# Kernel tuning notes

Hardware: AMD Instinct MI355X
Metric: run time of the kernel (lower is better)

The kernel has to match this reference:

```python
import jax, jax.numpy as jnp
import numpy as np

H = 16        # num_heads
E = 1024      # embed_size
OUT = 1024    # out_dim
TEMP = 1.0
EPS = 1e-20
LN_EPS = 1e-5


def setup_inputs() -> dict:
    key = jax.random.key(0)
    ks = jax.random.split(key, 16)
    B, S = 8, 4096
    s = 1.0 / np.sqrt(E)
    inp = {
        'x': jax.random.normal(ks[0], (B, S, E), dtype=jnp.float32),
        'gumbel_u': jax.random.uniform(ks[1], (B, H, S, 2), dtype=jnp.float32, minval=1e-6, maxval=1.0 - 1e-6),
        'query': jax.random.uniform(ks[2], (1, E), dtype=jnp.float32, minval=-s, maxval=s),  # xavier-ish
        'Wq': jax.random.uniform(ks[3], (E, E), jnp.float32, -s, s),
        'bq': jnp.zeros((E,), jnp.float32),
        'Wk': jax.random.uniform(ks[4], (E, E), jnp.float32, -s, s),
        'bk': jnp.zeros((E,), jnp.float32),
        'Wv': jax.random.uniform(ks[5], (E, E), jnp.float32, -s, s),
        'bv': jnp.zeros((E,), jnp.float32),
        'ln_g': jnp.ones((E,), jnp.float32),
        'ln_b': jnp.zeros((E,), jnp.float32),
        'W1': jax.random.uniform(ks[6], (4 * E, E), jnp.float32, -s, s),
        'b1': jnp.zeros((4 * E,), jnp.float32),
        'W2': jax.random.uniform(ks[7], (OUT, 4 * E), jnp.float32, -0.5 * s, 0.5 * s),
        'b2': jnp.zeros((OUT,), jnp.float32),
    }
    return inp


def reference(x, gumbel_u, query, Wq, bq, Wk, bk, Wv, bv, ln_g, ln_b, W1, b1, W2, b2):
    B, S, _ = x.shape
    dk = E // H
    # projections
    q = (query @ Wq.T + bq).reshape(H, dk)                      # [H, dk] (single query, broadcast over batch)
    k = (x @ Wk.T + bk).reshape(B, S, H, dk)                    # [B, S, H, dk]
    v = (x @ Wv.T + bv).reshape(B, S, H, dk)
    # single-query attention logits
    logits = jnp.einsum('hd,bshd->bhs', q, k) / np.sqrt(dk)     # [B, H, S]
    probs = jax.nn.softmax(logits, axis=-1)                     # [B, H, S]
    # gumbel-softmax hard mask over {keep=0-logit, drop/keep pair}
    edges = jnp.stack([jnp.zeros_like(logits), logits], axis=-1)  # [B, H, S, 2]
    g = -jnp.log(-jnp.log(gumbel_u + EPS) + EPS)
    y_soft = jax.nn.softmax((edges + g) / TEMP, axis=-1)
    idx = jnp.argmax(y_soft, axis=-1)
    y_hard = jax.nn.one_hot(idx, 2, dtype=y_soft.dtype)
    y = jax.lax.stop_gradient(y_hard - y_soft) + y_soft         # straight-through
    A = y[..., 1]                                               # [B, H, S]
    probs = A * probs
    # weighted sum of values; merge heads (seq_len of query is 1)
    hidden = jnp.einsum('bhs,bshd->bhd', probs, v).reshape(B, E)
    # layernorm
    mu = hidden.mean(axis=-1, keepdims=True)
    var = hidden.var(axis=-1, keepdims=True)
    hidden = (hidden - mu) / jnp.sqrt(var + LN_EPS) * ln_g + ln_b
    # MLP (dropout p=0 -> identity)
    out = jax.nn.relu(hidden @ W1.T + b1) @ W2.T + b2           # [B, OUT]
    masks = A.sum(axis=1)[:, None, :]                           # sum_heads=True -> [B, 1, S]
    attn = probs.sum(axis=1)[:, None, :]
    return out, masks, attn
```

## Files before the change

kernel.cpp:

```cpp
#include <hip/hip_runtime.h>
#include <hip/hip_bf16.h>
#include <math.h>

#define SS 4096
#define EE 1024
#define HH 16

typedef __bf16 bf16x8 __attribute__((ext_vector_type(8)));
typedef float  f32x4v __attribute__((ext_vector_type(4)));

#define OFF_QVEC 0L
#define OFF_QKB  1024L
#define OFF_QH   1040L
#define OFF_QL   9232L
#define OFF_SEC  17424L
#define OFF_SAC  50192L
#define OFF_INVD 82960L
#define OFF_PSUM 83088L
#define OFF_WG   83216L
#define OFF_XA   607504L
#define OFF_HID  738576L
#define OFF_H2   746768L
#define OFF_T1   754960L
#define OFF_PT   787728L
#define OFF_PX   820496L

__device__ __forceinline__ float bf2f(unsigned int u){
  union { unsigned int i; float f; } c; c.i = u << 16; return c.f;
}
__device__ __forceinline__ unsigned int pk_hi(float a, float b){
  return __builtin_amdgcn_perm(__float_as_uint(b), __float_as_uint(a), 0x07060302u);
}
__device__ __forceinline__ float lo_part(float f){
  return f - __uint_as_float(__float_as_uint(f) & 0xFFFF0000u);
}
__device__ __forceinline__ unsigned short f2bf_rn(float f){
  unsigned int u = __float_as_uint(f);
  return (unsigned short)((u + 0x7fffu + ((u >> 16) & 1u)) >> 16);
}
__device__ __forceinline__ f32x4v mfma16(bf16x8 a, bf16x8 b, f32x4v c){
  return __builtin_amdgcn_mfma_f32_16x16x32_bf16(a, b, c, 0, 0, 0);
}
__device__ __forceinline__ float waveRedSum(float v){
  #pragma unroll
  for (int m=1;m<64;m<<=1) v += __shfl_xor(v, m, 64);
  return v;
}
template<int NW>
__device__ __forceinline__ float blockRedSum(float v, volatile float* scr){
  v = waveRedSum(v);
  const int w = threadIdx.x >> 6;
  __syncthreads();
  if ((threadIdx.x & 63) == 0) scr[w] = v;
  __syncthreads();
  float r = 0.f;
  #pragma unroll
  for (int i=0;i<NW;i++) r += scr[i];
  return r;
}

__global__ __launch_bounds__(256) void k1(const float* __restrict__ query, const float* __restrict__ Wq,
                                          const float* __restrict__ bq, float* __restrict__ qvec){
  const int wv = threadIdx.x >> 6, lane = threadIdx.x & 63;
  const int j = blockIdx.x * 4 + wv;
  float p = 0.f;
  #pragma unroll
  for (int i=0;i<4;i++){
    const int e = 4*lane + 256*i;
    const float4 q4 = *(const float4*)(query + e);
    const float4 w4 = *(const float4*)(Wq + (long)j*EE + e);
    p += q4.x*w4.x + q4.y*w4.y + q4.z*w4.z + q4.w*w4.w;
  }
  p = waveRedSum(p);
  if (lane == 0) qvec[j] = p + bq[j];
}

__global__ __launch_bounds__(256) void k2(const float* __restrict__ Wk, const float* __restrict__ bk,
                                          const float* __restrict__ qvec,
                                          unsigned short* __restrict__ qh, unsigned short* __restrict__ ql,
                                          float* __restrict__ qkb){
  __shared__ float red[4][64];
  const int wv = threadIdx.x >> 6, lane = threadIdx.x & 63;
  const int h = blockIdx.y;
  const int e = blockIdx.x*64 + lane;
  float acc = 0.f;
  #pragma unroll
  for (int dd=0; dd<16; dd++){
    const int d = wv*16 + dd;
    acc += qvec[h*64+d] * Wk[(long)(h*64+d)*EE + e];
  }
  red[wv][lane] = acc;
  __syncthreads();
  if (wv == 0){
    const float s = red[0][lane] + red[1][lane] + red[2][lane] + red[3][lane];
    const unsigned int ub = __float_as_uint(s);
    qh[h*EE + e] = (unsigned short)(ub >> 16);
    const float lo = s - __uint_as_float(ub & 0xFFFF0000u);
    ql[h*EE + e] = (unsigned short)(__float_as_uint(lo) >> 16);
    if (blockIdx.x == 0){
      float p = qvec[h*64+lane] * bk[h*64+lane];
      p = waveRedSum(p);
      if (lane == 0) qkb[h] = p;
    }
  }
}

__global__ __launch_bounds__(256,2) void k3(const float* __restrict__ x, const float* __restrict__ gum,
                                            const unsigned short* __restrict__ qh, const unsigned short* __restrict__ ql,
                                            const float* __restrict__ qkb,
                                            float* __restrict__ seC, float* __restrict__ saC,
                                            float* __restrict__ Wg, float* __restrict__ out){
  __shared__ float lg[4*16*17];
  __shared__ float w[16*20];
  __shared__ float scrA[16*17], scrB[16*17];
  __shared__ float sQkb[16];
  const int t = threadIdx.x;
  const int wv = t >> 6, lane = t & 63;
  const int m16 = lane & 15, q = lane >> 4;
  const int c = blockIdx.x, b = blockIdx.y;
  if (t < 16) sQkb[t] = qkb[t];
  const long xbase = ((long)(b*SS + c*16))*EE;

  f32x4v a = {0.f,0.f,0.f,0.f};
  #pragma unroll
  for (int kt=0; kt<8; kt++){
    const int k = wv*256 + kt*32 + q*8;
    const float* xp = x + xbase + (long)m16*EE + k;
    const float4 f0 = *(const float4*)(xp);
    const float4 f1 = *(const float4*)(xp + 4);
    union { uint4 u; bf16x8 v; } xh, xl, bh, bl;
    xh.u.x = pk_hi(f0.x, f0.y); xh.u.y = pk_hi(f0.z, f0.w);
    xh.u.z = pk_hi(f1.x, f1.y); xh.u.w = pk_hi(f1.z, f1.w);
    xl.u.x = pk_hi(lo_part(f0.x), lo_part(f0.y)); xl.u.y = pk_hi(lo_part(f0.z), lo_part(f0.w));
    xl.u.z = pk_hi(lo_part(f1.x), lo_part(f1.y)); xl.u.w = pk_hi(lo_part(f1.z), lo_part(f1.w));
    bh.u = *(const uint4*)(qh + (long)m16*EE + k);
    bl.u = *(const uint4*)(ql + (long)m16*EE + k);
    a = mfma16(xh.v, bh.v, a);
    a = mfma16(xh.v, bl.v, a);
    a = mfma16(xl.v, bh.v, a);
  }
  #pragma unroll
  for (int r=0;r<4;r++)
    lg[(wv*16 + q*4 + r)*17 + m16] = a[r];
  __syncthreads();

  {
    const int h = t & 15, s = t >> 4;
    const float dot = lg[(0*16+s)*17+h] + lg[(1*16+s)*17+h]
                    + lg[(2*16+s)*17+h] + lg[(3*16+s)*17+h];
    const float logit = (dot + sQkb[h]) * 0.125f;
    const long gi = ((long)(b*16 + h))*SS + c*16 + s;
    const float2 g2 = *(const float2*)(gum + 2*gi);
    const double gg0 = -log(-log((double)g2.x + 1e-20) + 1e-20);
    const double gg1 = -log(-log((double)g2.y + 1e-20) + 1e-20);
    const float e = expf(logit);
    const float wval = ((double)logit + gg1 > gg0) ? e : 0.f;
    w[s*20 + h] = wval;
    Wg[((long)b*SS + c*16 + s)*16 + h] = wval;
    scrA[s*17 + h] = e;
    scrB[s*17 + h] = wval;
  }
  __syncthreads();
  if (t < 16){
    float S = 0.f, SA = 0.f, cnt = 0.f;
    #pragma unroll
    for (int i=0;i<16;i++){ S += scrA[i*17 + t]; SA += scrB[i*17 + t]; }
    #pragma unroll
    for (int hh=0; hh<16; hh++) cnt += (w[t*20 + hh] > 0.f) ? 1.f : 0.f;
    seC[((long)(b*16 + t))*256 + c] = S;
    saC[((long)(b*16 + t))*256 + c] = SA;
    out[8192 + (long)b*SS + c*16 + t] = cnt;
  }
}

__global__ __launch_bounds__(256) void k4(const float* __restrict__ seC, const float* __restrict__ saC,
                                          float* __restrict__ invD, float* __restrict__ psum){
  __shared__ float sA[16*17], sB[16*17];
  const int b = blockIdx.x, t = threadIdx.x;
  const int h = t >> 4, cl = t & 15;
  float se = 0.f, sa = 0.f;
  #pragma unroll
  for (int k=0;k<16;k++){
    se += seC[((long)(b*16+h))*256 + cl + 16*k];
    sa += saC[((long)(b*16+h))*256 + cl + 16*k];
  }
  sA[h*17+cl] = se; sB[h*17+cl] = sa;
  __syncthreads();
  if (t < 16){
    float D = 0.f, SA = 0.f;
    #pragma unroll
    for (int i=0;i<16;i++){ D += sA[t*17+i]; SA += sB[t*17+i]; }
    const float inv = 1.f / D;
    invD[b*16+t] = inv; psum[b*16+t] = SA * inv;
  }
}

__global__ __launch_bounds__(256) void k5agg(const float* __restrict__ x, const float* __restrict__ Wg,
                                             const float* __restrict__ invD,
                                             unsigned short* __restrict__ px, float* __restrict__ out){
  __shared__ float wl[64*20];
  __shared__ float sInv[16];
  const int t = threadIdx.x, sseg = blockIdx.x, b = blockIdx.y;
  if (t < 16) sInv[t] = invD[b*16 + t];
  const int s0 = sseg*64;
  const float4 wv4 = *(const float4*)(Wg + ((long)b*SS + s0)*16 + 4*t);
  *(float4*)&wl[(t>>2)*20 + 4*(t&3)] = wv4;
  __syncthreads();
  if (t < 64){
    float a = 0.f;
    #pragma unroll
    for (int h=0; h<16; h++) a += wl[t*20 + h] * sInv[h];
    out[40960 + (long)b*SS + s0 + t] = a;
  }
  float acc[16][4];
  #pragma unroll
  for (int hh=0; hh<16; hh++){ acc[hh][0]=0.f; acc[hh][1]=0.f; acc[hh][2]=0.f; acc[hh][3]=0.f; }
  const float* xp = x + ((long)(b*SS + s0))*EE + 4*t;
  #pragma unroll 2
  for (int s=0; s<64; s++){
    const float4 xf = *(const float4*)(xp + (long)s*EE);
    float wv[16];
    *(float4*)&wv[0]  = *(const float4*)&wl[s*20 + 0];
    *(float4*)&wv[4]  = *(const float4*)&wl[s*20 + 4];
    *(float4*)&wv[8]  = *(const float4*)&wl[s*20 + 8];
    *(float4*)&wv[12] = *(const float4*)&wl[s*20 + 12];
    #pragma unroll
    for (int hh=0; hh<16; hh++){
      acc[hh][0] += wv[hh]*xf.x; acc[hh][1] += wv[hh]*xf.y;
      acc[hh][2] += wv[hh]*xf.z; acc[hh][3] += wv[hh]*xf.w;
    }
  }
  #pragma unroll
  for (int hh=0; hh<16; hh++){
    uint2 pk;
    pk.x = ((unsigned int)f2bf_rn(acc[hh][0])) | (((unsigned int)f2bf_rn(acc[hh][1])) << 16);
    pk.y = ((unsigned int)f2bf_rn(acc[hh][2])) | (((unsigned int)f2bf_rn(acc[hh][3])) << 16);
    *(uint2*)(px + (((long)(b*64 + sseg))*16 + hh)*EE + 4*t) = pk;
  }
}

__global__ __launch_bounds__(256) void k5b(const unsigned short* __restrict__ px, float* __restrict__ xa){
  const long g = (long)blockIdx.x*512 + 2*threadIdx.x;
  const int e = (int)(g & 1023);
  const int bh = (int)(g >> 10);
  const int b = bh >> 4, h = bh & 15;
  const unsigned short* p = px + (((long)(b*64))*16 + h)*EE + e;
  float a0 = 0.f, a1 = 0.f;
  #pragma unroll 8
  for (int seg=0; seg<64; seg++){
    const unsigned int u = *(const unsigned int*)(p + (long)seg*16384);
    a0 += bf2f(u & 0xffffu); a1 += bf2f(u >> 16);
  }
  xa[g] = a0; xa[g+1] = a1;
}

__global__ __launch_bounds__(256) void k6a(const float* __restrict__ xa, const float* __restrict__ Wv,
                                           const float* __restrict__ bv, const float* __restrict__ invD,
                                           const float* __restrict__ psum, float* __restrict__ hid){
  const int wv = threadIdx.x >> 6, lane = threadIdx.x & 63;
  const int W = blockIdx.x*4 + wv;
  const int b = W >> 8, jg = (W & 255)*4;
  for (int jj=0; jj<4; jj++){
    const int j = jg + jj, h = j >> 6;
    const float* xr = xa + ((long)(b*16+h))*EE;
    const float* wr = Wv + (long)j*EE;
    float p = 0.f;
    #pragma unroll
    for (int i=0;i<4;i++){
      const int e = 4*lane + 256*i;
      const float4 a4 = *(const float4*)(xr + e);
      const float4 w4 = *(const float4*)(wr + e);
      p += a4.x*w4.x + a4.y*w4.y + a4.z*w4.z + a4.w*w4.w;
    }
    p = waveRedSum(p);
    if (lane == 0) hid[(long)b*EE + j] = p*invD[b*16+h] + psum[b*16+h]*bv[j];
  }
}

__global__ __launch_bounds__(1024) void k6b(const float* __restrict__ hid, const float* __restrict__ lng,
                                            const float* __restrict__ lnb, unsigned short* __restrict__ h2u){
  __shared__ float scr[16];
  const int b = blockIdx.x, t = threadIdx.x;
  if (b >= 8){ h2u[(long)b*EE + t] = 0; return; }
  const float v = hid[(long)b*EE + t];
  const float s1 = blockRedSum<16>(v, scr);
  const float s2 = blockRedSum<16>(v*v, scr);
  const float mu  = s1 * (1.f/1024.f);
  const float var = s2 * (1.f/1024.f) - mu*mu;
  const float rs = rsqrtf(var + 1e-5f);
  h2u[(long)b*EE + t] = f2bf_rn((v - mu)*rs*lng[t] + lnb[t]);
}

__global__ __launch_bounds__(256) void k8(const unsigned short* __restrict__ h2u, const float* __restrict__ W1,
                                          const float* __restrict__ b1, unsigned short* __restrict__ t1u){
  __shared__ float red[4*64*4];
  const int wv = threadIdx.x >> 6, lane = threadIdx.x & 63;
  const int m16 = lane & 15, q = lane >> 4;
  const int j = blockIdx.x*16 + m16;
  f32x4v a = {0.f,0.f,0.f,0.f};
  #pragma unroll
  for (int kt=0; kt<8; kt++){
    const int k = wv*256 + kt*32 + q*8;
    union { uint4 u; bf16x8 v; } A, B;
    A.u = *(const uint4*)(h2u + (long)m16*EE + k);
    const float4 f0 = *(const float4*)(W1 + (long)j*EE + k);
    const float4 f1 = *(const float4*)(W1 + (long)j*EE + k + 4);
    B.u.x = pk_hi(f0.x,f0.y); B.u.y = pk_hi(f0.z,f0.w);
    B.u.z = pk_hi(f1.x,f1.y); B.u.w = pk_hi(f1.z,f1.w);
    a = mfma16(A.v, B.v, a);
  }
  #pragma unroll
  for (int r=0;r<4;r++) red[(wv*64 + lane)*4 + r] = a[r];
  __syncthreads();
  if (wv == 0){
    #pragma unroll
    for (int r=0;r<4;r++){
      const float s = red[(0*64+lane)*4+r] + red[(1*64+lane)*4+r]
                    + red[(2*64+lane)*4+r] + red[(3*64+lane)*4+r];
      const int row = q*4 + r;
      const float val = (row < 8) ? fmaxf(s + b1[j], 0.f) : 0.f;
      t1u[(long)row*4096 + j] = f2bf_rn(val);
    }
  }
}

__global__ __launch_bounds__(256) void k9(const unsigned short* __restrict__ t1u, const float* __restrict__ W2,
                                          float* __restrict__ pt){
  __shared__ float red[4*64*4];
  const int wv = threadIdx.x >> 6, lane = threadIdx.x & 63;
  const int m16 = lane & 15, q = lane >> 4;
  const int o = blockIdx.x*16 + m16;
  const int kbase = blockIdx.y*1024 + wv*256;
  f32x4v a = {0.f,0.f,0.f,0.f};
  #pragma unroll
  for (int kt=0; kt<8; kt++){
    const int k = kbase + kt*32 + q*8;
    union { uint4 u; bf16x8 v; } A, B;
    A.u = *(const uint4*)(t1u + (long)m16*4096 + k);
    const float4 f0 = *(const float4*)(W2 + (long)o*4096 + k);
    const float4 f1 = *(const float4*)(W2 + (long)o*4096 + k + 4);
    B.u.x = pk_hi(f0.x,f0.y); B.u.y = pk_hi(f0.z,f0.w);
    B.u.z = pk_hi(f1.x,f1.y); B.u.w = pk_hi(f1.z,f1.w);
    a = mfma16(A.v, B.v, a);
  }
  #pragma unroll
  for (int r=0;r<4;r++) red[(wv*64 + lane)*4 + r] = a[r];
  __syncthreads();
  if (wv == 0){
    #pragma unroll
    for (int r=0;r<4;r++){
      const int row = q*4 + r;
      if (row < 8){
        const float s = red[(0*64+lane)*4+r] + red[(1*64+lane)*4+r]
                      + red[(2*64+lane)*4+r] + red[(3*64+lane)*4+r];
        pt[(long)blockIdx.y*8192 + row*1024 + o] = s;
      }
    }
  }
}

__global__ __launch_bounds__(256) void k9b(const float* __restrict__ pt, const float* __restrict__ b2,
                                           float* __restrict__ out){
  const int idx = blockIdx.x*256 + threadIdx.x;
  const int o = idx & 1023;
  out[idx] = pt[idx] + pt[8192+idx] + pt[16384+idx] + pt[24576+idx] + b2[o];
}

extern "C" void kernel_launch(void* const* d_in, const int* in_sizes, int n_in,
                              void* d_out, int out_size, void* d_ws, size_t ws_size,
                              hipStream_t stream){
  const float* x    = (const float*)d_in[0];
  const float* gum  = (const float*)d_in[1];
  const float* query= (const float*)d_in[2];
  const float* Wq   = (const float*)d_in[3];
  const float* bq   = (const float*)d_in[4];
  const float* Wk   = (const float*)d_in[5];
  const float* bk   = (const float*)d_in[6];
  const float* Wv   = (const float*)d_in[7];
  const float* bv   = (const float*)d_in[8];
  const float* lng  = (const float*)d_in[9];
  const float* lnb  = (const float*)d_in[10];
  const float* W1   = (const float*)d_in[11];
  const float* b1   = (const float*)d_in[12];
  const float* W2   = (const float*)d_in[13];
  const float* b2   = (const float*)d_in[14];
  float* ws = (float*)d_ws;
  float* qvec = ws + OFF_QVEC;
  float* qkb  = ws + OFF_QKB;
  unsigned short* qh = (unsigned short*)(ws + OFF_QH);
  unsigned short* ql = (unsigned short*)(ws + OFF_QL);
  float* seC  = ws + OFF_SEC;
  float* saC  = ws + OFF_SAC;
  float* invD = ws + OFF_INVD;
  float* psum = ws + OFF_PSUM;
  float* Wg   = ws + OFF_WG;
  float* xa   = ws + OFF_XA;
  float* hid  = ws + OFF_HID;
  unsigned short* h2u = (unsigned short*)(ws + OFF_H2);
  unsigned short* t1u = (unsigned short*)(ws + OFF_T1);
  float* pt   = ws + OFF_PT;
  unsigned short* px  = (unsigned short*)(ws + OFF_PX);
  float* out = (float*)d_out;

  k1   <<<256, 256, 0, stream>>>(query, Wq, bq, qvec);
  k2   <<<dim3(16,16), 256, 0, stream>>>(Wk, bk, qvec, qh, ql, qkb);
  k3   <<<dim3(256,8), 256, 0, stream>>>(x, gum, qh, ql, qkb, seC, saC, Wg, out);
  k4   <<<8, 256, 0, stream>>>(seC, saC, invD, psum);
  k5agg<<<dim3(64,8), 256, 0, stream>>>(x, Wg, invD, px, out);
  k5b  <<<256, 256, 0, stream>>>(px, xa);
  k6a  <<<512, 256, 0, stream>>>(xa, Wv, bv, invD, psum, hid);
  k6b  <<<16, 1024, 0, stream>>>(hid, lng, lnb, h2u);
  k8   <<<256, 256, 0, stream>>>(h2u, W1, b1, t1u);
  k9   <<<dim3(64,4), 256, 0, stream>>>(t1u, W2, pt);
  k9b  <<<32, 256, 0, stream>>>(pt, b2, out);
}
```

Baseline: 305.0 us.

## Fuse segment reduction into Wv projection and layernorm into W1 GEMM

Merges the px segment-reduction kernel into the Wv projection kernel, which now reduces one head's aggregated x row into shared memory and reuses it for its 16 output columns. Layernorm moves into the W1 MFMA kernel: each block recomputes the per-batch layernorm into LDS as bf16 rather than reading a global buffer. The k5agg x loop is also restructured to issue four row loads before the FMAs. The aim is to drop two launches and the global round trips, at the cost of each block redoing the layernorm and the 64-segment px reduction redundantly (px reads repeat 4x).

```diff
diff --git a/kernel.cpp b/kernel.cpp
--- a/kernel.cpp
+++ b/kernel.cpp
@@ -18,9 +18,7 @@
 #define OFF_INVD 82960L
 #define OFF_PSUM 83088L
 #define OFF_WG   83216L
-#define OFF_XA   607504L
 #define OFF_HID  738576L
-#define OFF_H2   746768L
 #define OFF_T1   754960L
 #define OFF_PT   787728L
 #define OFF_PX   820496L
@@ -216,18 +214,23 @@
   #pragma unroll
   for (int hh=0; hh<16; hh++){ acc[hh][0]=0.f; acc[hh][1]=0.f; acc[hh][2]=0.f; acc[hh][3]=0.f; }
   const float* xp = x + ((long)(b*SS + s0))*EE + 4*t;
-  #pragma unroll 2
-  for (int s=0; s<64; s++){
-    const float4 xf = *(const float4*)(xp + (long)s*EE);
-    float wv[16];
-    *(float4*)&wv[0]  = *(const float4*)&wl[s*20 + 0];
-    *(float4*)&wv[4]  = *(const float4*)&wl[s*20 + 4];
-    *(float4*)&wv[8]  = *(const float4*)&wl[s*20 + 8];
-    *(float4*)&wv[12] = *(const float4*)&wl[s*20 + 12];
-    #pragma unroll
-    for (int hh=0; hh<16; hh++){
-      acc[hh][0] += wv[hh]*xf.x; acc[hh][1] += wv[hh]*xf.y;
-      acc[hh][2] += wv[hh]*xf.z; acc[hh][3] += wv[hh]*xf.w;
+  for (int sb=0; sb<64; sb+=4){
+    float4 xf[4];
+    #pragma unroll
+    for (int i=0;i<4;i++) xf[i] = *(const float4*)(xp + (long)(sb+i)*EE);
+    #pragma unroll
+    for (int i=0;i<4;i++){
+      const int s = sb + i;
+      float wv[16];
+      *(float4*)&wv[0]  = *(const float4*)&wl[s*20 + 0];
+      *(float4*)&wv[4]  = *(const float4*)&wl[s*20 + 4];
+      *(float4*)&wv[8]  = *(const float4*)&wl[s*20 + 8];
+      *(float4*)&wv[12] = *(const float4*)&wl[s*20 + 12];
+      #pragma unroll
+      for (int hh=0; hh<16; hh++){
+        acc[hh][0] += wv[hh]*xf[i].x; acc[hh][1] += wv[hh]*xf[i].y;
+        acc[hh][2] += wv[hh]*xf[i].z; acc[hh][3] += wv[hh]*xf[i].w;
+      }
     }
   }
   #pragma unroll
@@ -239,70 +242,81 @@
   }
 }
 
-__global__ __launch_bounds__(256) void k5b(const unsigned short* __restrict__ px, float* __restrict__ xa){
-  const long g = (long)blockIdx.x*512 + 2*threadIdx.x;
-  const int e = (int)(g & 1023);
-  const int bh = (int)(g >> 10);
-  const int b = bh >> 4, h = bh & 15;
-  const unsigned short* p = px + (((long)(b*64))*16 + h)*EE + e;
-  float a0 = 0.f, a1 = 0.f;
-  #pragma unroll 8
-  for (int seg=0; seg<64; seg++){
-    const unsigned int u = *(const unsigned int*)(p + (long)seg*16384);
-    a0 += bf2f(u & 0xffffu); a1 += bf2f(u >> 16);
-  }
-  xa[g] = a0; xa[g+1] = a1;
-}
-
-__global__ __launch_bounds__(256) void k6a(const float* __restrict__ xa, const float* __restrict__ Wv,
-                                           const float* __restrict__ bv, const float* __restrict__ invD,
-                                           const float* __restrict__ psum, float* __restrict__ hid){
-  const int wv = threadIdx.x >> 6, lane = threadIdx.x & 63;
-  const int W = blockIdx.x*4 + wv;
-  const int b = W >> 8, jg = (W & 255)*4;
+__global__ __launch_bounds__(256) void k6(const unsigned short* __restrict__ px, const float* __restrict__ Wv,
+                                          const float* __restrict__ bv, const float* __restrict__ invD,
+                                          const float* __restrict__ psum, float* __restrict__ hid){
+  __shared__ float xas[1024];
+  const int t = threadIdx.x;
+  const int wv = t >> 6, lane = t & 63;
+  const int b = blockIdx.x >> 6;
+  const int jbase = (blockIdx.x & 63) * 16;
+  const int h = jbase >> 6;
+  {
+    float a0=0.f,a1=0.f,a2=0.f,a3=0.f;
+    const unsigned short* p = px + (((long)(b*64))*16 + h)*EE + 4*t;
+    #pragma unroll 8
+    for (int seg=0; seg<64; seg++){
+      const uint2 u = *(const uint2*)(p + (long)seg*16384);
+      a0 += bf2f(u.x & 0xffffu); a1 += bf2f(u.x >> 16);
+      a2 += bf2f(u.y & 0xffffu); a3 += bf2f(u.y >> 16);
+    }
+    *(float4*)&xas[4*t] = make_float4(a0,a1,a2,a3);
+  }
+  __syncthreads();
+  const float iD = invD[b*16+h], ps = psum[b*16+h];
+  const int jg = jbase + wv*4;
   for (int jj=0; jj<4; jj++){
-    const int j = jg + jj, h = j >> 6;
-    const float* xr = xa + ((long)(b*16+h))*EE;
+    const int j = jg + jj;
     const float* wr = Wv + (long)j*EE;
     float p = 0.f;
     #pragma unroll
     for (int i=0;i<4;i++){
       const int e = 4*lane + 256*i;
-      const float4 a4 = *(const float4*)(xr + e);
+      const float4 a4 = *(const float4*)&xas[e];
       const float4 w4 = *(const float4*)(wr + e);
       p += a4.x*w4.x + a4.y*w4.y + a4.z*w4.z + a4.w*w4.w;
     }
     p = waveRedSum(p);
-    if (lane == 0) hid[(long)b*EE + j] = p*invD[b*16+h] + psum[b*16+h]*bv[j];
-  }
-}
-
-__global__ __launch_bounds__(1024) void k6b(const float* __restrict__ hid, const float* __restrict__ lng,
-                                            const float* __restrict__ lnb, unsigned short* __restrict__ h2u){
-  __shared__ float scr[16];
-  const int b = blockIdx.x, t = threadIdx.x;
-  if (b >= 8){ h2u[(long)b*EE + t] = 0; return; }
-  const float v = hid[(long)b*EE + t];
-  const float s1 = blockRedSum<16>(v, scr);
-  const float s2 = blockRedSum<16>(v*v, scr);
-  const float mu  = s1 * (1.f/1024.f);
-  const float var = s2 * (1.f/1024.f) - mu*mu;
-  const float rs = rsqrtf(var + 1e-5f);
-  h2u[(long)b*EE + t] = f2bf_rn((v - mu)*rs*lng[t] + lnb[t]);
-}
-
-__global__ __launch_bounds__(256) void k8(const unsigned short* __restrict__ h2u, const float* __restrict__ W1,
+    if (lane == 0) hid[(long)b*EE + j] = p*iD + ps*bv[j];
+  }
+}
+
+__global__ __launch_bounds__(256) void k8(const float* __restrict__ hid, const float* __restrict__ lng,
+                                          const float* __restrict__ lnb, const float* __restrict__ W1,
                                           const float* __restrict__ b1, unsigned short* __restrict__ t1u){
+  __shared__ unsigned short h2s[16*1024];
   __shared__ float red[4*64*4];
-  const int wv = threadIdx.x >> 6, lane = threadIdx.x & 63;
+  __shared__ float scr[4];
+  const int t = threadIdx.x;
+  const int wv = t >> 6, lane = t & 63;
   const int m16 = lane & 15, q = lane >> 4;
+  #pragma unroll
+  for (int i=0;i<16;i++) ((unsigned int*)h2s)[4096 + t + 256*i] = 0u;
+  const float4 g4  = *(const float4*)(lng + 4*t);
+  const float4 bb4 = *(const float4*)(lnb + 4*t);
+  for (int b=0; b<8; b++){
+    const float4 v4 = *(const float4*)(hid + (long)b*EE + 4*t);
+    float s1 = v4.x+v4.y+v4.z+v4.w;
+    float s2 = v4.x*v4.x+v4.y*v4.y+v4.z*v4.z+v4.w*v4.w;
+    s1 = blockRedSum<4>(s1, scr);
+    s2 = blockRedSum<4>(s2, scr);
+    const float mu  = s1*(1.f/1024.f);
+    const float var = s2*(1.f/1024.f) - mu*mu;
+    const float rs  = rsqrtf(var + 1e-5f);
+    unsigned short* dst = h2s + b*1024 + 4*t;
+    dst[0] = f2bf_rn((v4.x-mu)*rs*g4.x + bb4.x);
+    dst[1] = f2bf_rn((v4.y-mu)*rs*g4.y + bb4.y);
+    dst[2] = f2bf_rn((v4.z-mu)*rs*g4.z + bb4.z);
+    dst[3] = f2bf_rn((v4.w-mu)*rs*g4.w + bb4.w);
+  }
+  __syncthreads();
   const int j = blockIdx.x*16 + m16;
   f32x4v a = {0.f,0.f,0.f,0.f};
   #pragma unroll
   for (int kt=0; kt<8; kt++){
     const int k = wv*256 + kt*32 + q*8;
     union { uint4 u; bf16x8 v; } A, B;
-    A.u = *(const uint4*)(h2u + (long)m16*EE + k);
+    A.u = *(const uint4*)(h2s + (long)m16*1024 + k);
     const float4 f0 = *(const float4*)(W1 + (long)j*EE + k);
     const float4 f1 = *(const float4*)(W1 + (long)j*EE + k + 4);
     B.u.x = pk_hi(f0.x,f0.y); B.u.y = pk_hi(f0.z,f0.w);
@@ -394,9 +408,7 @@
   float* invD = ws + OFF_INVD;
   float* psum = ws + OFF_PSUM;
   float* Wg   = ws + OFF_WG;
-  float* xa   = ws + OFF_XA;
   float* hid  = ws + OFF_HID;
-  unsigned short* h2u = (unsigned short*)(ws + OFF_H2);
   unsigned short* t1u = (unsigned short*)(ws + OFF_T1);
   float* pt   = ws + OFF_PT;
   unsigned short* px  = (unsigned short*)(ws + OFF_PX);
@@ -407,10 +419,8 @@
   k3   <<<dim3(256,8), 256, 0, stream>>>(x, gum, qh, ql, qkb, seC, saC, Wg, out);
   k4   <<<8, 256, 0, stream>>>(seC, saC, invD, psum);
   k5agg<<<dim3(64,8), 256, 0, stream>>>(x, Wg, invD, px, out);
-  k5b  <<<256, 256, 0, stream>>>(px, xa);
-  k6a  <<<512, 256, 0, stream>>>(xa, Wv, bv, invD, psum, hid);
-  k6b  <<<16, 1024, 0, stream>>>(hid, lng, lnb, h2u);
-  k8   <<<256, 256, 0, stream>>>(h2u, W1, b1, t1u);
+  k6   <<<512, 256, 0, stream>>>(px, Wv, bv, invD, psum, hid);
+  k8   <<<256, 256, 0, stream>>>(hid, lng, lnb, W1, b1, t1u);
   k9   <<<dim3(64,4), 256, 0, stream>>>(t1u, W2, pt);
   k9b  <<<32, 256, 0, stream>>>(pt, b2, out);
 }
```

New measurement: 313.6 us. 1.03x slower.
